# Kernel tuning notes

Hardware: AMD Instinct MI355X
Metric: run time of the kernel (lower is better)

The kernel has to match this reference:

```python
import jax, jax.numpy as jnp
import numpy as np

N = 50000   # nodes
E = 600000  # edges
D = 128     # input_dim
H = 128     # hidden_dim
K = 2       # num_layers (propagation hops)


def setup_inputs() -> dict:
    key = jax.random.key(0)
    k1, k2, k3 = jax.random.split(key, 3)
    x = jax.random.normal(k1, (N, D), dtype=jnp.float32)
    edge_index = jax.random.randint(k2, (2, E), 0, N, dtype=jnp.int64)
    # Linear(input_dim -> hidden_dim) params (PyG default: glorot-ish weight, zero bias)
    W = jax.random.normal(k3, (H, D), dtype=jnp.float32) / np.float32(np.sqrt(D))
    b = jnp.zeros((H,), dtype=jnp.float32)
    return {"x": x, "edge_index": edge_index, "W": W, "b": b}


def reference(x, edge_index, W, b):
    n = x.shape[0]
    loop = jnp.arange(n, dtype=edge_index.dtype)
    # gcn_norm: add self-loops with weight 1, symmetric normalization
    row = jnp.concatenate([edge_index[0], loop])  # source nodes
    col = jnp.concatenate([edge_index[1], loop])  # target nodes
    w = jnp.ones(row.shape[0], dtype=x.dtype)
    deg = jax.ops.segment_sum(w, col, num_segments=n)
    dinv = jnp.where(deg > 0, jax.lax.rsqrt(deg), jnp.zeros_like(deg))
    norm = dinv[row] * w * dinv[col]  # [E+N]
    # K hops of normalized sparse propagation: x <- A_hat @ x
    for _ in range(K):
        x = jax.ops.segment_sum(norm[:, None] * x[row], col, num_segments=n)
    # Linear projection + activation
    z = x @ W.T + b
    return jax.nn.relu(z)
```

## Files before the change

kernel.cpp:

```cpp
#include <hip/hip_runtime.h>

#define D 128
#define CAP 128
#define NR 8
typedef unsigned int uint;
typedef unsigned short ushort;
typedef __attribute__((ext_vector_type(8))) short bf16x8;
typedef __attribute__((ext_vector_type(4))) float f32x4;

__device__ __forceinline__ float2 bf2_to_f2(uint v) {
    union { uint u; float f; } a, b;
    a.u = v << 16;
    b.u = v & 0xffff0000u;
    return make_float2(a.f, b.f);
}
__device__ __forceinline__ uint f2_to_bf2(float x, float y) {
    uint xu = __float_as_uint(x), yu = __float_as_uint(y);
    xu += 0x7fffu + ((xu >> 16) & 1u);
    yu += 0x7fffu + ((yu >> 16) & 1u);
    return (xu >> 16) | (yu & 0xffff0000u);
}

__device__ __forceinline__ void sum8(const uint* __restrict__ zin, const int* __restrict__ lst,
                                     int k, int lane, float2& acc) {
    int r0 = lst[k],     r1 = lst[k + 1], r2 = lst[k + 2], r3 = lst[k + 3];
    int r4 = lst[k + 4], r5 = lst[k + 5], r6 = lst[k + 6], r7 = lst[k + 7];
    uint v0 = zin[(size_t)r0 * 64 + lane], v1 = zin[(size_t)r1 * 64 + lane];
    uint v2 = zin[(size_t)r2 * 64 + lane], v3 = zin[(size_t)r3 * 64 + lane];
    uint v4 = zin[(size_t)r4 * 64 + lane], v5 = zin[(size_t)r5 * 64 + lane];
    uint v6 = zin[(size_t)r6 * 64 + lane], v7 = zin[(size_t)r7 * 64 + lane];
    float2 f0 = bf2_to_f2(v0), f1 = bf2_to_f2(v1), f2 = bf2_to_f2(v2), f3 = bf2_to_f2(v3);
    float2 f4 = bf2_to_f2(v4), f5 = bf2_to_f2(v5), f6 = bf2_to_f2(v6), f7 = bf2_to_f2(v7);
    acc.x += ((f0.x + f1.x) + (f2.x + f3.x)) + ((f4.x + f5.x) + (f6.x + f7.x));
    acc.y += ((f0.y + f1.y) + (f2.y + f3.y)) + ((f4.y + f5.y) + (f6.y + f7.y));
}

__global__ __launch_bounds__(256) void edge_build_kernel(
        const int* __restrict__ ei, int E, int n,
        int* __restrict__ deg, int* __restrict__ slots,
        const float* __restrict__ W, uint* __restrict__ Wbf,
        uint* __restrict__ zX, uint* __restrict__ zB, int edgeB) {
    int b = blockIdx.x, t = threadIdx.x;
    if (b < edgeB) {
        int range = b & (NR - 1);
        int e = (b >> 3) * 256 + t;
        if (e < E) {
            int c = ei[E + e];
            int per = (n + NR - 1) / NR;
            int lo = range * per;
            if (c >= lo && c < lo + per) {
                int r = ei[e];
                int pos = atomicAdd(&deg[c], 1);
                if (pos < CAP) slots[(size_t)c * CAP + pos] = r;
            }
        }
    } else if (b < edgeB + ((D * D / 2) + 255) / 256) {
        int i = (b - edgeB) * 256 + t;
        if (i < (D * D) / 2) {
            float2 wv = ((const float2*)W)[i];
            Wbf[i] = f2_to_bf2(wv.x, wv.y);
        }
    } else {
        if (t < 64) {
            zX[(size_t)n * 64 + t] = 0u;
            zB[(size_t)n * 64 + t] = 0u;
        }
    }
}

__global__ __launch_bounds__(256) void scale_cast_kernel(
        const float* __restrict__ x, const int* __restrict__ deg,
        int* __restrict__ slots, uint2* __restrict__ zX, int n) {
    int idx = blockIdx.x * 256 + threadIdx.x;
    if (idx < n * 32) {
        int node = idx >> 5;
        float dv = rsqrtf((float)(deg[node] + 1));
        float4 v = ((const float4*)x)[idx];
        uint2 o;
        o.x = f2_to_bf2(v.x * dv, v.y * dv);
        o.y = f2_to_bf2(v.z * dv, v.w * dv);
        zX[idx] = o;
        if ((idx & 31) == 0) {
            int len = deg[node]; if (len > CAP) len = CAP;
            int len8 = (len + 7) & ~7;
            for (int j = len; j < len8; ++j) slots[(size_t)node * CAP + j] = n;
        }
    }
}

template<bool HOP1>
__global__ __launch_bounds__(256) void prop_kernel(const uint* __restrict__ zin,
                                                   uint* __restrict__ zout,
                                                   const int* __restrict__ deg,
                                                   const int* __restrict__ slots,
                                                   int n) {
    int wv = threadIdx.x >> 6, lane = threadIdx.x & 63;
    int c = blockIdx.x * 4 + wv;
    if (c >= n) return;
    int len = deg[c]; if (len > CAP) len = CAP;
    int len8 = (len + 7) & ~7;
    const int* lst = slots + (size_t)c * CAP;
    size_t selfoff = (size_t)c * 64 + lane;
    float2 acc = bf2_to_f2(zin[selfoff]);
    for (int k = 0; k < len8; k += 8) sum8(zin, lst, k, lane, acc);
    float s = rsqrtf((float)(len + 1));
    float sc = HOP1 ? s * s : s;
    zout[selfoff] = f2_to_bf2(acc.x * sc, acc.y * sc);
}

#define GN 64
__global__ __launch_bounds__(256) void gemm_mfma(const uint4* __restrict__ x2,
                                                 const uint4* __restrict__ Wbf,
                                                 const float* __restrict__ bias,
                                                 float* __restrict__ out, int n) {
    __shared__ __align__(16) ushort xs[GN][136];
    __shared__ __align__(16) ushort ws[D][136];
    int t = threadIdx.x;
    int n0 = blockIdx.x * GN;
    for (int i = t; i < D * 16; i += 256) {
        int row = i >> 4, c8 = i & 15;
        uint4 v = Wbf[i];
        *(uint4*)&ws[row][c8 * 8] = v;
    }
    for (int i = t; i < GN * 16; i += 256) {
        int row = i >> 4, c8 = i & 15;
        int node = n0 + row;
        uint4 v = (node < n) ? x2[(size_t)node * 16 + c8] : make_uint4(0u, 0u, 0u, 0u);
        *(uint4*)&xs[row][c8 * 8] = v;
    }
    __syncthreads();

    int w = t >> 6, lane = t & 63;
    int m0 = w * 16;
    int mrow = lane & 15, quad = lane >> 4;

    bf16x8 a[4];
#pragma unroll
    for (int q = 0; q < 4; ++q)
        a[q] = *(const bf16x8*)&xs[m0 + mrow][q * 32 + quad * 8];

    f32x4 acc[8];
#pragma unroll
    for (int ht = 0; ht < 8; ++ht) {
        acc[ht] = (f32x4){0.f, 0.f, 0.f, 0.f};
#pragma unroll
        for (int q = 0; q < 4; ++q) {
            bf16x8 bfr = *(const bf16x8*)&ws[ht * 16 + mrow][q * 32 + quad * 8];
            acc[ht] = __builtin_amdgcn_mfma_f32_16x16x32_bf16(a[q], bfr, acc[ht], 0, 0, 0);
        }
    }

#pragma unroll
    for (int ht = 0; ht < 8; ++ht) {
        int h = ht * 16 + mrow;
        float bv = bias[h];
#pragma unroll
        for (int reg = 0; reg < 4; ++reg) {
            int node = n0 + m0 + quad * 4 + reg;
            if (node < n)
                out[(size_t)node * D + h] = fmaxf(acc[ht][reg] + bv, 0.f);
        }
    }
}

extern "C" void kernel_launch(void* const* d_in, const int* in_sizes, int n_in,
                              void* d_out, int out_size, void* d_ws, size_t ws_size,
                              hipStream_t stream) {
    const float* x  = (const float*)d_in[0];
    const int*   ei = (const int*)d_in[1];
    const float* W  = (const float*)d_in[2];
    const float* bias = (const float*)d_in[3];
    float* out = (float*)d_out;
    int N = in_sizes[0] / D;
    int E = in_sizes[1] / 2;

    char* p = (char*)d_ws;
    auto alloc = [&](size_t bytes) -> void* {
        void* r = p; p += (bytes + 511) & ~(size_t)511; return r;
    };
    int*    deg     = (int*)alloc((size_t)N * 4);
    int*    slots   = (int*)alloc((size_t)N * CAP * 4);
    uint*   zX      = (uint*)alloc((size_t)(N + 1) * 64 * 4);
    uint*   zB      = (uint*)alloc((size_t)(N + 1) * 64 * 4);
    uint*   zA      = (uint*)alloc((size_t)N * 64 * 4);
    uint*   Wbf     = (uint*)alloc((size_t)(D * D / 2) * 4);

    int edgeB = ((E + 255) / 256) * NR;
    int wB    = ((D * D / 2) + 255) / 256;
    int xB    = (N * 32 + 255) / 256;

    hipMemsetAsync(deg, 0, (size_t)N * 4, stream);
    edge_build_kernel<<<edgeB + wB + 1, 256, 0, stream>>>(ei, E, N, deg, slots, W, Wbf,
                                                          zX, zB, edgeB);
    scale_cast_kernel<<<xB, 256, 0, stream>>>(x, deg, slots, (uint2*)zX, N);
    prop_kernel<true ><<<(N + 3) / 4, 256, 0, stream>>>(zX, zB, deg, slots, N);
    prop_kernel<false><<<(N + 3) / 4, 256, 0, stream>>>(zB, zA, deg, slots, N);
    gemm_mfma<<<(N + GN - 1) / GN, 256, 0, stream>>>((const uint4*)zA, (const uint4*)Wbf, bias, out, N);
}
```

Measured before the change: 180.1 us.

## Split features into XCD-pinned quarters, shrink neighbour slots to ushort cap 64

Features are stored as four feature-quarter planes. Propagation blocks are remapped so that each pair of XCDs (assumed from blockIdx mod 8) gathers only one quarter, which cuts each XCD's gather working set to fit its local L2. Neighbour indices become 16-bit with a cap of 64, and nontemporal loads and stores are added. The ushort index truncates node ids above 65535, which is fine for N=50000. The cap of 64 could drop edges for high-degree nodes, though with a mean degree of about 12 that is very unlikely.

```diff
diff --git a/kernel.cpp b/kernel.cpp
--- a/kernel.cpp
+++ b/kernel.cpp
@@ -1,7 +1,7 @@
 #include <hip/hip_runtime.h>
 
 #define D 128
-#define CAP 128
+#define CAP 64
 #define NR 8
 typedef unsigned int uint;
 typedef unsigned short ushort;
@@ -21,25 +21,11 @@
     return (xu >> 16) | (yu & 0xffff0000u);
 }
 
-__device__ __forceinline__ void sum8(const uint* __restrict__ zin, const int* __restrict__ lst,
-                                     int k, int lane, float2& acc) {
-    int r0 = lst[k],     r1 = lst[k + 1], r2 = lst[k + 2], r3 = lst[k + 3];
-    int r4 = lst[k + 4], r5 = lst[k + 5], r6 = lst[k + 6], r7 = lst[k + 7];
-    uint v0 = zin[(size_t)r0 * 64 + lane], v1 = zin[(size_t)r1 * 64 + lane];
-    uint v2 = zin[(size_t)r2 * 64 + lane], v3 = zin[(size_t)r3 * 64 + lane];
-    uint v4 = zin[(size_t)r4 * 64 + lane], v5 = zin[(size_t)r5 * 64 + lane];
-    uint v6 = zin[(size_t)r6 * 64 + lane], v7 = zin[(size_t)r7 * 64 + lane];
-    float2 f0 = bf2_to_f2(v0), f1 = bf2_to_f2(v1), f2 = bf2_to_f2(v2), f3 = bf2_to_f2(v3);
-    float2 f4 = bf2_to_f2(v4), f5 = bf2_to_f2(v5), f6 = bf2_to_f2(v6), f7 = bf2_to_f2(v7);
-    acc.x += ((f0.x + f1.x) + (f2.x + f3.x)) + ((f4.x + f5.x) + (f6.x + f7.x));
-    acc.y += ((f0.y + f1.y) + (f2.y + f3.y)) + ((f4.y + f5.y) + (f6.y + f7.y));
-}
-
 __global__ __launch_bounds__(256) void edge_build_kernel(
         const int* __restrict__ ei, int E, int n,
-        int* __restrict__ deg, int* __restrict__ slots,
+        int* __restrict__ deg, ushort* __restrict__ slots,
         const float* __restrict__ W, uint* __restrict__ Wbf,
-        uint* __restrict__ zX, uint* __restrict__ zB, int edgeB) {
+        uint* __restrict__ zXq, uint* __restrict__ zBq, int edgeB) {
     int b = blockIdx.x, t = threadIdx.x;
     if (b < edgeB) {
         int range = b & (NR - 1);
@@ -51,7 +37,7 @@
             if (c >= lo && c < lo + per) {
                 int r = ei[e];
                 int pos = atomicAdd(&deg[c], 1);
-                if (pos < CAP) slots[(size_t)c * CAP + pos] = r;
+                if (pos < CAP) slots[(size_t)c * CAP + pos] = (ushort)r;
             }
         }
     } else if (b < edgeB + ((D * D / 2) + 255) / 256) {
@@ -62,28 +48,31 @@
         }
     } else {
         if (t < 64) {
-            zX[(size_t)n * 64 + t] = 0u;
-            zB[(size_t)n * 64 + t] = 0u;
+            int q = t >> 4, u = t & 15;
+            size_t off = ((size_t)q * (n + 1) + n) * 16 + u;
+            zXq[off] = 0u;
+            zBq[off] = 0u;
         }
     }
 }
 
 __global__ __launch_bounds__(256) void scale_cast_kernel(
         const float* __restrict__ x, const int* __restrict__ deg,
-        int* __restrict__ slots, uint2* __restrict__ zX, int n) {
+        ushort* __restrict__ slots, uint* __restrict__ zXq, int n) {
     int idx = blockIdx.x * 256 + threadIdx.x;
     if (idx < n * 32) {
         int node = idx >> 5;
+        int j = idx & 31;
+        int q = j >> 3, ju = j & 7;
         float dv = rsqrtf((float)(deg[node] + 1));
         float4 v = ((const float4*)x)[idx];
-        uint2 o;
-        o.x = f2_to_bf2(v.x * dv, v.y * dv);
-        o.y = f2_to_bf2(v.z * dv, v.w * dv);
-        zX[idx] = o;
+        size_t base = ((size_t)q * (n + 1) + node) * 16 + ju * 2;
+        __builtin_nontemporal_store(f2_to_bf2(v.x * dv, v.y * dv), &zXq[base]);
+        __builtin_nontemporal_store(f2_to_bf2(v.z * dv, v.w * dv), &zXq[base + 1]);
         if ((idx & 31) == 0) {
             int len = deg[node]; if (len > CAP) len = CAP;
             int len8 = (len + 7) & ~7;
-            for (int j = len; j < len8; ++j) slots[(size_t)node * CAP + j] = n;
+            for (int jj = len; jj < len8; ++jj) slots[(size_t)node * CAP + jj] = (ushort)n;
         }
     }
 }
@@ -92,20 +81,43 @@
 __global__ __launch_bounds__(256) void prop_kernel(const uint* __restrict__ zin,
                                                    uint* __restrict__ zout,
                                                    const int* __restrict__ deg,
-                                                   const int* __restrict__ slots,
+                                                   const ushort* __restrict__ slots,
                                                    int n) {
-    int wv = threadIdx.x >> 6, lane = threadIdx.x & 63;
-    int c = blockIdx.x * 4 + wv;
+    int b = blockIdx.x;
+    int xcd = b & 7;
+    int q = xcd >> 1;
+    int chunk = (b >> 3) * 2 + (xcd & 1);
+    int lane = threadIdx.x & 63, w = threadIdx.x >> 6;
+    int g = lane >> 4, u = lane & 15;
+    int c = chunk * 16 + w * 4 + g;
     if (c >= n) return;
     int len = deg[c]; if (len > CAP) len = CAP;
     int len8 = (len + 7) & ~7;
-    const int* lst = slots + (size_t)c * CAP;
-    size_t selfoff = (size_t)c * 64 + lane;
-    float2 acc = bf2_to_f2(zin[selfoff]);
-    for (int k = 0; k < len8; k += 8) sum8(zin, lst, k, lane, acc);
+    const ushort* lst = slots + (size_t)c * CAP;
+    const uint* zq = zin + (size_t)q * (n + 1) * 16;
+    uint* zoq = zout + (size_t)q * (n + 1) * 16;
+    float2 acc = bf2_to_f2(zq[(size_t)c * 16 + u]);
+    for (int k = 0; k < len8; k += 8) {
+        int r0 = __builtin_nontemporal_load(&lst[k]);
+        int r1 = __builtin_nontemporal_load(&lst[k + 1]);
+        int r2 = __builtin_nontemporal_load(&lst[k + 2]);
+        int r3 = __builtin_nontemporal_load(&lst[k + 3]);
+        int r4 = __builtin_nontemporal_load(&lst[k + 4]);
+        int r5 = __builtin_nontemporal_load(&lst[k + 5]);
+        int r6 = __builtin_nontemporal_load(&lst[k + 6]);
+        int r7 = __builtin_nontemporal_load(&lst[k + 7]);
+        uint v0 = zq[(size_t)r0 * 16 + u], v1 = zq[(size_t)r1 * 16 + u];
+        uint v2 = zq[(size_t)r2 * 16 + u], v3 = zq[(size_t)r3 * 16 + u];
+        uint v4 = zq[(size_t)r4 * 16 + u], v5 = zq[(size_t)r5 * 16 + u];
+        uint v6 = zq[(size_t)r6 * 16 + u], v7 = zq[(size_t)r7 * 16 + u];
+        float2 f0 = bf2_to_f2(v0), f1 = bf2_to_f2(v1), f2 = bf2_to_f2(v2), f3 = bf2_to_f2(v3);
+        float2 f4 = bf2_to_f2(v4), f5 = bf2_to_f2(v5), f6 = bf2_to_f2(v6), f7 = bf2_to_f2(v7);
+        acc.x += ((f0.x + f1.x) + (f2.x + f3.x)) + ((f4.x + f5.x) + (f6.x + f7.x));
+        acc.y += ((f0.y + f1.y) + (f2.y + f3.y)) + ((f4.y + f5.y) + (f6.y + f7.y));
+    }
     float s = rsqrtf((float)(len + 1));
     float sc = HOP1 ? s * s : s;
-    zout[selfoff] = f2_to_bf2(acc.x * sc, acc.y * sc);
+    __builtin_nontemporal_store(f2_to_bf2(acc.x * sc, acc.y * sc), &zoq[(size_t)c * 16 + u]);
 }
 
 #define GN 64
@@ -125,7 +137,9 @@
     for (int i = t; i < GN * 16; i += 256) {
         int row = i >> 4, c8 = i & 15;
         int node = n0 + row;
-        uint4 v = (node < n) ? x2[(size_t)node * 16 + c8] : make_uint4(0u, 0u, 0u, 0u);
+        int q = c8 >> 2, r4 = c8 & 3;
+        uint4 v = (node < n) ? x2[((size_t)q * (n + 1) + node) * 4 + r4]
+                             : make_uint4(0u, 0u, 0u, 0u);
         *(uint4*)&xs[row][c8 * 8] = v;
     }
     __syncthreads();
@@ -179,21 +193,23 @@
         void* r = p; p += (bytes + 511) & ~(size_t)511; return r;
     };
     int*    deg     = (int*)alloc((size_t)N * 4);
-    int*    slots   = (int*)alloc((size_t)N * CAP * 4);
-    uint*   zX      = (uint*)alloc((size_t)(N + 1) * 64 * 4);
-    uint*   zB      = (uint*)alloc((size_t)(N + 1) * 64 * 4);
-    uint*   zA      = (uint*)alloc((size_t)N * 64 * 4);
+    ushort* slots   = (ushort*)alloc((size_t)N * CAP * 2);
+    uint*   zXq     = (uint*)alloc((size_t)4 * (N + 1) * 16 * 4);
+    uint*   zBq     = (uint*)alloc((size_t)4 * (N + 1) * 16 * 4);
+    uint*   zAq     = (uint*)alloc((size_t)4 * (N + 1) * 16 * 4);
     uint*   Wbf     = (uint*)alloc((size_t)(D * D / 2) * 4);
 
     int edgeB = ((E + 255) / 256) * NR;
     int wB    = ((D * D / 2) + 255) / 256;
     int xB    = (N * 32 + 255) / 256;
+    int chunks16 = (N + 15) / 16;
+    int propB = ((chunks16 + 1) / 2) * 8;
 
     hipMemsetAsync(deg, 0, (size_t)N * 4, stream);
     edge_build_kernel<<<edgeB + wB + 1, 256, 0, stream>>>(ei, E, N, deg, slots, W, Wbf,
-                                                          zX, zB, edgeB);
-    scale_cast_kernel<<<xB, 256, 0, stream>>>(x, deg, slots, (uint2*)zX, N);
-    prop_kernel<true ><<<(N + 3) / 4, 256, 0, stream>>>(zX, zB, deg, slots, N);
-    prop_kernel<false><<<(N + 3) / 4, 256, 0, stream>>>(zB, zA, deg, slots, N);
-    gemm_mfma<<<(N + GN - 1) / GN, 256, 0, stream>>>((const uint4*)zA, (const uint4*)Wbf, bias, out, N);
-}
+                                                          zXq, zBq, edgeB);
+    scale_cast_kernel<<<xB, 256, 0, stream>>>(x, deg, slots, zXq, N);
+    prop_kernel<true ><<<propB, 256, 0, stream>>>(zXq, zBq, deg, slots, N);
+    prop_kernel<false><<<propB, 256, 0, stream>>>(zBq, zAq, deg, slots, N);
+    gemm_mfma<<<(N + GN - 1) / GN, 256, 0, stream>>>((const uint4*)zAq, (const uint4*)Wbf, bias, out, N);
+}
```

Measured after the change: 201.3 us. +11.8%, slower.
